# Kernel tuning notes

Hardware: AMD Instinct MI355X
Metric: run time of the kernel (lower is better)

Reference implementation:

```python
import jax, jax.numpy as jnp
import numpy as np


def setup_inputs() -> dict:
    key = jax.random.key(0)
    k1, k2 = jax.random.split(key)
    x = jax.random.normal(k1, (16, 128, 64, 64), dtype=jnp.float32)
    # weight layout: [out_channels, in_channels, kh, kw], kernel must be 3 for the
    # original Python-loop bounds to match the allocated output size
    weight = jax.random.normal(k2, (256, 128, 3, 3), dtype=jnp.float32) * 0.05
    return {"x": x, "weight": weight}


def reference(x, weight):
    # Stride-1 conv2d with symmetric zero padding=1 (forward ignores bias/stride/
    # dilation/groups in the original module).
    pad = 1
    out = jax.lax.conv_general_dilated(
        x, weight,
        window_strides=(1, 1),
        padding=[(pad, pad), (pad, pad)],
        dimension_numbers=("NCHW", "OIHW", "NCHW"),
    )
    return out
```

## Files before the change

kernel.cpp:

```cpp
#include <hip/hip_runtime.h>
#include <hip/hip_bf16.h>
#include <stdint.h>

typedef short bf16x8 __attribute__((ext_vector_type(8)));
typedef float f32x16 __attribute__((ext_vector_type(16)));

#define N_IMG 16
#define C_IN  128
#define H_IMG 64
#define W_IMG 64
#define K_OUT 256

#define XB_BYTES (16ull*66*66*128*2)
#define WB_BYTES (9ull*256*128*2)
#define WS_NEED  (XB_BYTES + WB_BYTES)

#define LDSX_BYTES (6*66*256)
#define WCH_BYTES  16384
#define LDS_TOTAL  (LDSX_BYTES + 3*WCH_BYTES)

__device__ __forceinline__ void gload16(void* lds, const void* g) {
    __builtin_amdgcn_global_load_lds(
        (const __attribute__((address_space(1))) void*)g,
        (__attribute__((address_space(3))) void*)lds, 16, 0, 0);
}

__global__ void transform_w_kernel(const float* __restrict__ w,
                                   __hip_bfloat16* __restrict__ wb) {
    __shared__ float lw[1152];
    const int kg = blockIdx.x;
    const int t  = threadIdx.x;
    for (int e = t; e < 1152; e += 256) lw[e] = w[kg * 1152 + e];
    __syncthreads();
    for (int e = t; e < 1152; e += 256) {
        int tap = e >> 7;
        int c   = e & 127;
        wb[(tap * 256 + kg) * 128 + c] = __float2bfloat16(lw[c * 9 + tap]);
    }
}

__device__ __forceinline__ uint32_t pack2(float a, float b) {
    __hip_bfloat16 ha = __float2bfloat16(a), hb = __float2bfloat16(b);
    return (uint32_t)*(uint16_t*)&ha | ((uint32_t)*(uint16_t*)&hb << 16);
}

__global__ void transform_x_kernel(const float* __restrict__ x,
                                   __hip_bfloat16* __restrict__ xb) {
    __shared__ __align__(16) uint32_t xsT[64 * 68];
    const int b  = blockIdx.x;
    const int yt = b % 66;
    const int n  = b / 66;
    const int t  = threadIdx.x;
    const bool interior = (yt >= 1 && yt <= 64);

    if (interior) {
        const float4* src = (const float4*)(x + (size_t)n * 524288 + (size_t)(yt - 1) * 64);
        #pragma unroll
        for (int it = 0; it < 4; ++it) {
            int e  = t + it * 256;
            int c2 = e >> 4;
            int x4 = e & 15;
            float4 va = src[(2 * c2) * 1024 + x4];
            float4 vb = src[(2 * c2 + 1) * 1024 + x4];
            int xr = x4 * 4;
            xsT[(xr + 0) * 68 + c2] = pack2(va.x, vb.x);
            xsT[(xr + 1) * 68 + c2] = pack2(va.y, vb.y);
            xsT[(xr + 2) * 68 + c2] = pack2(va.z, vb.z);
            xsT[(xr + 3) * 68 + c2] = pack2(va.w, vb.w);
        }
    }
    __syncthreads();

    uint4* dst = (uint4*)((char*)xb + (size_t)(n * 66 + yt) * 66 * 256);
    for (int ch = t; ch < 1056; ch += 256) {
        int xt = ch >> 4;
        int cp = ch & 15;
        uint4 val = make_uint4(0u, 0u, 0u, 0u);
        if (interior && xt >= 1 && xt <= 64)
            val = *(const uint4*)&xsT[(xt - 1) * 68 + cp * 4];
        dst[ch] = val;
    }
}

__global__ __launch_bounds__(512, 2)
void conv3x3_mfma_kernel(const char* __restrict__ xg,
                         const char* __restrict__ wg,
                         float* __restrict__ out) {
    __shared__ uint4 smem[LDS_TOTAL / 16];
    char* lds  = (char*)smem;
    char* ldsW = lds + LDSX_BYTES;

    const int t    = threadIdx.x;
    const int b    = blockIdx.x;
    const int q    = b & 15;
    const int n    = b >> 4;
    const int lane = t & 63;
    const int wv   = t >> 6;
    const int lm   = lane & 31;
    const int hi   = lane >> 5;
    const int kb   = (wv >> 1) * 64;
    const int mb   = (wv & 1) * 128;

    int addrW[2][2];
    #pragma unroll
    for (int kf = 0; kf < 2; ++kf) {
        int krow = kb + kf * 32 + lm;
        #pragma unroll
        for (int ks = 0; ks < 2; ++ks)
            addrW[kf][ks] = krow * 64 + ((ks * 32 + hi * 16) ^ ((krow & 3) << 4));
    }
    int rc0[4];
    #pragma unroll
    for (int f = 0; f < 4; ++f) {
        int m = mb + f * 32 + lm;
        rc0[f] = (m >> 6) * 66 + (m & 63);
    }
    const int coffX0 = hi * 16;

    const int krow0 = t >> 2;
    const int woffA = krow0 * 256 + (((t & 3) ^ (krow0 & 3)) << 4);

    const char* xsrc = xg + (size_t)(n * 66 + q * 4) * 66 * 256;
    for (int ch = t; ch < 6336; ch += 512) {
        int L = ch * 16;
        gload16(lds + L, xsrc + (L ^ (((L >> 8) & 7) << 4)));
    }
    #pragma unroll
    for (int jj = 0; jj < 2; ++jj) {
        const char* s = wg + (jj >> 2) * 65536 + (jj & 3) * 64;
        char* d = ldsW + jj * WCH_BYTES + t * 16;
        gload16(d, s + woffA);
        gload16(d + 8192, s + woffA + 32768);
    }
    asm volatile("s_waitcnt vmcnt(2)" ::: "memory");
    __builtin_amdgcn_sched_barrier(0);
    __builtin_amdgcn_s_barrier();

    f32x16 acc[2][4];
    #pragma unroll
    for (int i = 0; i < 2; ++i)
        #pragma unroll
        for (int j = 0; j < 4; ++j)
            acc[i][j] = (f32x16)(0.f);

    int bR = 0;
    int bP = 2;
    for (int j = 0; j < 36; ++j) {
        {
            int jj = j + 2; if (jj >= 36) jj -= 36;
            int tap2 = jj >> 2, cc2 = jj & 3;
            const char* s = wg + tap2 * 65536 + cc2 * 64;
            char* d = ldsW + bP * WCH_BYTES + t * 16;
            gload16(d, s + woffA);
            gload16(d + 8192, s + woffA + 32768);
        }
        const int tap = j >> 2;
        const int cc  = j & 3;
        const int r   = (tap >= 6) ? 2 : (tap >= 3 ? 1 : 0);
        const int s_  = tap - r * 3;
        const int rs66 = r * 66 + s_;
        const char* wbuf = ldsW + bR * WCH_BYTES;

        __builtin_amdgcn_s_setprio(1);
        #pragma unroll
        for (int ks = 0; ks < 2; ++ks) {
            bf16x8 a0 = *(const bf16x8*)(wbuf + addrW[0][ks]);
            bf16x8 a1 = *(const bf16x8*)(wbuf + addrW[1][ks]);
            const int co = cc * 64 + ks * 32 + coffX0;
            #pragma unroll
            for (int f = 0; f < 4; ++f) {
                int rc = rc0[f] + rs66;
                int L  = rc * 256 + (co ^ ((rc & 7) << 4));
                bf16x8 bfr = *(const bf16x8*)(lds + L);
                acc[0][f] = __builtin_amdgcn_mfma_f32_32x32x16_bf16(a0, bfr, acc[0][f], 0, 0, 0);
                acc[1][f] = __builtin_amdgcn_mfma_f32_32x32x16_bf16(a1, bfr, acc[1][f], 0, 0, 0);
            }
        }
        __builtin_amdgcn_s_setprio(0);

        asm volatile("s_waitcnt vmcnt(2)" ::: "memory");
        __builtin_amdgcn_sched_barrier(0);
        __builtin_amdgcn_s_barrier();

        bR = (bR == 2) ? 0 : bR + 1;
        bP = (bP == 2) ? 0 : bP + 1;
    }

    const int y0 = q * 4;
    #pragma unroll
    for (int kf = 0; kf < 2; ++kf) {
        const int kbase2 = kb + kf * 32 + 4 * hi;
        #pragma unroll
        for (int f = 0; f < 4; ++f) {
            int m  = mb + f * 32 + lm;
            int yy = m >> 6;
            int xx = m & 63;
            float* op = out + (((size_t)(n * 256 + kbase2) * 64) + y0 + yy) * 64 + xx;
            #pragma unroll
            for (int reg = 0; reg < 16; ++reg) {
                int koff = (reg & 3) + 8 * (reg >> 2);
                op[(size_t)koff * 4096] = acc[kf][f][reg];
            }
        }
    }
}

__global__ __launch_bounds__(256, 3)
void conv3x3_f32_kernel(const float* __restrict__ x,
                        const float* __restrict__ w,
                        float* __restrict__ out) {
    __shared__ float xs[16][3][72];
    __shared__ float ws[16][9][64];

    const int t  = threadIdx.x;
    const int kt = blockIdx.x & 3;
    const int y  = (blockIdx.x >> 2) & 63;
    const int n  = blockIdx.x >> 8;

    const int k2   = t >> 3;
    const int xg   = t & 7;
    const int kloc = k2 * 2;
    const int x0   = xg * 8;

    float acc0[8] = {0.f,0.f,0.f,0.f,0.f,0.f,0.f,0.f};
    float acc1[8] = {0.f,0.f,0.f,0.f,0.f,0.f,0.f,0.f};

    const int k0 = kt * 64;

    for (int c0 = 0; c0 < C_IN; c0 += 16) {
        for (int idx = t; idx < 16 * 3 * 66; idx += 256) {
            int col = idx % 66;
            int rc  = idx / 66;
            int r   = rc % 3;
            int c   = rc / 3;
            int gx  = col - 1;
            int gy  = y - 1 + r;
            float v = 0.f;
            if ((unsigned)gx < (unsigned)W_IMG && (unsigned)gy < (unsigned)H_IMG)
                v = x[(((n * C_IN) + c0 + c) * H_IMG + gy) * W_IMG + gx];
            xs[c][r][col] = v;
        }
        for (int idx = t; idx < 64 * 16 * 9; idx += 256) {
            int tap = idx % 9;
            int ck  = idx / 9;
            int c   = ck % 16;
            int k   = ck / 16;
            ws[c][tap][k] = w[((k0 + k) * C_IN + c0 + c) * 9 + tap];
        }
        __syncthreads();

        #pragma unroll 2
        for (int c = 0; c < 16; ++c) {
            #pragma unroll
            for (int r = 0; r < 3; ++r) {
                float xr[10];
                #pragma unroll
                for (int i = 0; i < 10; ++i) xr[i] = xs[c][r][x0 + i];
                #pragma unroll
                for (int s = 0; s < 3; ++s) {
                    float w0 = ws[c][r * 3 + s][kloc];
                    float w1 = ws[c][r * 3 + s][kloc + 1];
                    #pragma unroll
                    for (int i = 0; i < 8; ++i) {
                        acc0[i] = fmaf(w0, xr[i + s], acc0[i]);
                        acc1[i] = fmaf(w1, xr[i + s], acc1[i]);
                    }
                }
            }
        }
        __syncthreads();
    }

    float* o0 = &out[(((n * K_OUT) + k0 + kloc) * H_IMG + y) * W_IMG + x0];
    float* o1 = o0 + H_IMG * W_IMG;
    #pragma unroll
    for (int i = 0; i < 8; ++i) o0[i] = acc0[i];
    #pragma unroll
    for (int i = 0; i < 8; ++i) o1[i] = acc1[i];
}

extern "C" void kernel_launch(void* const* d_in, const int* in_sizes, int n_in,
                              void* d_out, int out_size, void* d_ws, size_t ws_size,
                              hipStream_t stream) {
    const float* x = (const float*)d_in[0];
    const float* w = (const float*)d_in[1];
    float* out = (float*)d_out;
    (void)in_sizes; (void)n_in; (void)out_size;

    if (ws_size >= WS_NEED) {
        __hip_bfloat16* xb = (__hip_bfloat16*)d_ws;
        __hip_bfloat16* wb = (__hip_bfloat16*)((char*)d_ws + XB_BYTES);
        transform_w_kernel<<<256, 256, 0, stream>>>(w, wb);
        transform_x_kernel<<<16 * 66, 256, 0, stream>>>(x, xb);
        conv3x3_mfma_kernel<<<256, 512, 0, stream>>>((const char*)xb, (const char*)wb, out);
    } else {
        conv3x3_f32_kernel<<<4096, 256, 0, stream>>>(x, w, out);
    }
}
```

Before: 135.0 us.

## Fuse input/weight transforms into one launch and software-pipeline LDS reads of input fragments

Merges the weight and input bf16 transform kernels into a single launch, removing one kernel launch and its dependency gap. The input transpose's LDS tile changes from padding to an XOR swizzle. In the main MFMA loop, the input B-fragments for the next chunk are read from LDS while the current chunk's MFMAs run, using two ping-ponged register sets. This hides LDS latency behind the MFMAs but raises register pressure at launch bounds of 512 threads with 2 blocks per CU, which could cause spills or lower occupancy.

```diff
diff --git a/kernel.cpp b/kernel.cpp
--- a/kernel.cpp
+++ b/kernel.cpp
@@ -25,60 +25,68 @@
         (__attribute__((address_space(3))) void*)lds, 16, 0, 0);
 }
 
-__global__ void transform_w_kernel(const float* __restrict__ w,
-                                   __hip_bfloat16* __restrict__ wb) {
-    __shared__ float lw[1152];
-    const int kg = blockIdx.x;
-    const int t  = threadIdx.x;
-    for (int e = t; e < 1152; e += 256) lw[e] = w[kg * 1152 + e];
-    __syncthreads();
-    for (int e = t; e < 1152; e += 256) {
-        int tap = e >> 7;
-        int c   = e & 127;
-        wb[(tap * 256 + kg) * 128 + c] = __float2bfloat16(lw[c * 9 + tap]);
-    }
-}
-
 __device__ __forceinline__ uint32_t pack2(float a, float b) {
     __hip_bfloat16 ha = __float2bfloat16(a), hb = __float2bfloat16(b);
     return (uint32_t)*(uint16_t*)&ha | ((uint32_t)*(uint16_t*)&hb << 16);
 }
 
-__global__ void transform_x_kernel(const float* __restrict__ x,
-                                   __hip_bfloat16* __restrict__ xb) {
-    __shared__ __align__(16) uint32_t xsT[64 * 68];
-    const int b  = blockIdx.x;
-    const int yt = b % 66;
-    const int n  = b / 66;
-    const int t  = threadIdx.x;
-    const bool interior = (yt >= 1 && yt <= 64);
-
-    if (interior) {
-        const float4* src = (const float4*)(x + (size_t)n * 524288 + (size_t)(yt - 1) * 64);
-        #pragma unroll
-        for (int it = 0; it < 4; ++it) {
-            int e  = t + it * 256;
-            int c2 = e >> 4;
-            int x4 = e & 15;
-            float4 va = src[(2 * c2) * 1024 + x4];
-            float4 vb = src[(2 * c2 + 1) * 1024 + x4];
-            int xr = x4 * 4;
-            xsT[(xr + 0) * 68 + c2] = pack2(va.x, vb.x);
-            xsT[(xr + 1) * 68 + c2] = pack2(va.y, vb.y);
-            xsT[(xr + 2) * 68 + c2] = pack2(va.z, vb.z);
-            xsT[(xr + 3) * 68 + c2] = pack2(va.w, vb.w);
-        }
-    }
-    __syncthreads();
-
-    uint4* dst = (uint4*)((char*)xb + (size_t)(n * 66 + yt) * 66 * 256);
-    for (int ch = t; ch < 1056; ch += 256) {
-        int xt = ch >> 4;
-        int cp = ch & 15;
-        uint4 val = make_uint4(0u, 0u, 0u, 0u);
-        if (interior && xt >= 1 && xt <= 64)
-            val = *(const uint4*)&xsT[(xt - 1) * 68 + cp * 4];
-        dst[ch] = val;
+__global__ __launch_bounds__(256)
+void transform_fused_kernel(const float* __restrict__ x, const float* __restrict__ w,
+                            __hip_bfloat16* __restrict__ xb, __hip_bfloat16* __restrict__ wb) {
+    __shared__ __align__(16) uint32_t xs[64 * 64];
+    const int b = blockIdx.x;
+    const int t = threadIdx.x;
+
+    if (b < 1056) {
+        const int yt = b % 66;
+        const int n  = b / 66;
+        const bool interior = (yt >= 1 && yt <= 64);
+
+        if (interior) {
+            const float4* src = (const float4*)(x + (size_t)n * 524288 + (size_t)(yt - 1) * 64);
+            #pragma unroll
+            for (int it = 0; it < 4; ++it) {
+                const int x4 = t & 15;
+                const int j  = (t >> 4) + it * 16;
+                float4 va = src[(2 * j) * 1024 + x4];
+                float4 vb = src[(2 * j + 1) * 1024 + x4];
+                const float* pa = (const float*)&va;
+                const float* pb = (const float*)&vb;
+                #pragma unroll
+                for (int i = 0; i < 4; ++i) {
+                    int row = x4 * 4 + i;
+                    xs[row * 64 + (j ^ (((row >> 2) & 3) << 2))] = pack2(pa[i], pb[i]);
+                }
+            }
+        }
+        __syncthreads();
+
+        uint4* dst = (uint4*)((char*)xb + (size_t)(n * 66 + yt) * 66 * 256);
+        #pragma unroll
+        for (int it = 0; it < 5; ++it) {
+            int ch = t + it * 256;
+            if (ch < 1056) {
+                int xt = ch >> 4, u = ch & 15;
+                uint4 val = make_uint4(0u, 0u, 0u, 0u);
+                if (interior && xt >= 1 && xt <= 64) {
+                    int row = xt - 1;
+                    val = *(const uint4*)&xs[row * 64 + 4 * (u ^ ((row >> 2) & 3))];
+                }
+                dst[ch] = val;
+            }
+        }
+    } else {
+        const int kg = b - 1056;
+        #pragma unroll
+        for (int it = 0; it < 5; ++it) {
+            int e = t + it * 256;
+            if (e < 1152) {
+                int tap = e >> 7;
+                int c   = e & 127;
+                wb[(tap * 256 + kg) * 128 + c] =
+                    __float2bfloat16(w[kg * 1152 + c * 9 + tap]);
+            }
+        }
     }
 }
 
@@ -115,7 +123,6 @@
         int m = mb + f * 32 + lm;
         rc0[f] = (m >> 6) * 66 + (m & 63);
     }
-    const int coffX0 = hi * 16;
 
     const int krow0 = t >> 2;
     const int woffA = krow0 * 256 + (((t & 3) ^ (krow0 & 3)) << 4);
@@ -145,35 +152,50 @@
 
     int bR = 0;
     int bP = 2;
-    for (int j = 0; j < 36; ++j) {
+
+    auto loadx = [&](bf16x8 (&X)[2][4], int jj) {
+        int tap = jj >> 2, cc = jj & 3;
+        int r   = (tap >= 6) ? 2 : (tap >= 3 ? 1 : 0);
+        int s_  = tap - r * 3;
+        int rs66 = r * 66 + s_;
+        #pragma unroll
+        for (int ks = 0; ks < 2; ++ks) {
+            const int co = cc * 64 + ks * 32 + hi * 16;
+            #pragma unroll
+            for (int f = 0; f < 4; ++f) {
+                int rc = rc0[f] + rs66;
+                int L  = rc * 256 + (co ^ ((rc & 7) << 4));
+                X[ks][f] = *(const bf16x8*)(lds + L);
+            }
+        }
+    };
+
+    auto chunk = [&](int j, bf16x8 (&XC)[2][4], bf16x8 (&XN)[2][4]) {
+        int jj2 = j + 2; if (jj2 >= 36) jj2 -= 36;
         {
-            int jj = j + 2; if (jj >= 36) jj -= 36;
-            int tap2 = jj >> 2, cc2 = jj & 3;
+            int tap2 = jj2 >> 2, cc2 = jj2 & 3;
             const char* s = wg + tap2 * 65536 + cc2 * 64;
             char* d = ldsW + bP * WCH_BYTES + t * 16;
             gload16(d, s + woffA);
             gload16(d + 8192, s + woffA + 32768);
         }
-        const int tap = j >> 2;
-        const int cc  = j & 3;
-        const int r   = (tap >= 6) ? 2 : (tap >= 3 ? 1 : 0);
-        const int s_  = tap - r * 3;
-        const int rs66 = r * 66 + s_;
         const char* wbuf = ldsW + bR * WCH_BYTES;
+        bf16x8 a[2][2];
+        #pragma unroll
+        for (int kf = 0; kf < 2; ++kf)
+            #pragma unroll
+            for (int ks = 0; ks < 2; ++ks)
+                a[kf][ks] = *(const bf16x8*)(wbuf + addrW[kf][ks]);
+        int jn = j + 1; if (jn >= 36) jn -= 36;
+        loadx(XN, jn);
 
         __builtin_amdgcn_s_setprio(1);
         #pragma unroll
         for (int ks = 0; ks < 2; ++ks) {
-            bf16x8 a0 = *(const bf16x8*)(wbuf + addrW[0][ks]);
-            bf16x8 a1 = *(const bf16x8*)(wbuf + addrW[1][ks]);
-            const int co = cc * 64 + ks * 32 + coffX0;
             #pragma unroll
             for (int f = 0; f < 4; ++f) {
-                int rc = rc0[f] + rs66;
-                int L  = rc * 256 + (co ^ ((rc & 7) << 4));
-                bf16x8 bfr = *(const bf16x8*)(lds + L);
-                acc[0][f] = __builtin_amdgcn_mfma_f32_32x32x16_bf16(a0, bfr, acc[0][f], 0, 0, 0);
-                acc[1][f] = __builtin_amdgcn_mfma_f32_32x32x16_bf16(a1, bfr, acc[1][f], 0, 0, 0);
+                acc[0][f] = __builtin_amdgcn_mfma_f32_32x32x16_bf16(a[0][ks], XC[ks][f], acc[0][f], 0, 0, 0);
+                acc[1][f] = __builtin_amdgcn_mfma_f32_32x32x16_bf16(a[1][ks], XC[ks][f], acc[1][f], 0, 0, 0);
             }
         }
         __builtin_amdgcn_s_setprio(0);
@@ -184,6 +206,13 @@
 
         bR = (bR == 2) ? 0 : bR + 1;
         bP = (bP == 2) ? 0 : bP + 1;
+    };
+
+    bf16x8 xA[2][4], xB[2][4];
+    loadx(xA, 0);
+    for (int j = 0; j < 36; j += 2) {
+        chunk(j,     xA, xB);
+        chunk(j + 1, xB, xA);
     }
 
     const int y0 = q * 4;
@@ -290,8 +319,7 @@
     if (ws_size >= WS_NEED) {
         __hip_bfloat16* xb = (__hip_bfloat16*)d_ws;
         __hip_bfloat16* wb = (__hip_bfloat16*)((char*)d_ws + XB_BYTES);
-        transform_w_kernel<<<256, 256, 0, stream>>>(w, wb);
-        transform_x_kernel<<<16 * 66, 256, 0, stream>>>(x, xb);
+        transform_fused_kernel<<<1056 + 256, 256, 0, stream>>>(x, w, xb, wb);
         conv3x3_mfma_kernel<<<256, 512, 0, stream>>>((const char*)xb, (const char*)wb, out);
     } else {
         conv3x3_f32_kernel<<<4096, 256, 0, stream>>>(x, w, out);
```

Measured after the change: 132.9 us. About the same (-1.6%).
